# Performance work log

Hardware: AMD Instinct MI355X
Metric: run time of the kernel (lower is better)

The kernel has to match this reference:

```python
import jax, jax.numpy as jnp
import numpy as np

B, S, H, L = 16, 512, 768, 4096

def setup_inputs() -> dict:
    key = jax.random.key(0)
    k1, k2, k3 = jax.random.split(key, 3)
    inputs = jax.random.normal(k1, (B, S, H), dtype=jnp.float32)
    # realistic variable-length masks: each sequence has length in [S//2, S]
    lengths = jax.random.randint(k2, (B,), S // 2, S + 1)
    masks = jnp.arange(S)[None, :] < lengths[:, None]  # [B, S] bool
    # xavier_uniform for Linear(H, L, bias=False): weight shape [L, H]
    limit = float(np.sqrt(6.0 / (H + L)))
    W = jax.random.uniform(k3, (L, H), minval=-limit, maxval=limit, dtype=jnp.float32)
    return {"inputs": inputs, "masks": masks, "W": W}

def reference(inputs, masks, W):
    # scores: Linear(inputs) -> [B,S,L], transposed to [B,L,S]
    scores = jnp.einsum("bsh,lh->bls", inputs, W)
    scores = jnp.where(masks[:, None, :], scores, -jnp.inf)
    attn = jax.nn.softmax(scores, axis=-1)  # over seq dim
    # weighted sum pooling: [B,L,S] @ [B,S,H] -> [B,L,H]
    return jnp.einsum("bls,bsh->blh", attn, inputs)
```

## Files before the change

### kernel.cpp

```cpp
#include <hip/hip_runtime.h>
#include <hip/hip_bf16.h>

#define Bn 16
#define Sn 512
#define Hn 768
#define Ln 4096

typedef __attribute__((ext_vector_type(8))) short bf16x8;
typedef __attribute__((ext_vector_type(4))) float f32x4;

using bf16 = __hip_bfloat16;

constexpr int BL = 64;

constexpr int SM_BYTES = 81920;
constexpr int XS_OFF   = 0;
constexpr int WS_OFF   = 32768;
constexpr int P_OFF    = 0;
constexpr int XT_OFF   = 65536;
constexpr int REDM_OFF = 65536;
constexpr int REDS_OFF = 66048;

typedef const __attribute__((address_space(1))) unsigned int* gas_ptr;
typedef __attribute__((address_space(3))) unsigned int* las_ptr;

__device__ __forceinline__ void gld_lds16(const void* g, void* l) {
  __builtin_amdgcn_global_load_lds((gas_ptr)g, (las_ptr)l, 16, 0, 0);
}

__device__ __forceinline__ unsigned short bfbits(float x) {
  __hip_bfloat16 h = __float2bfloat16(x);
  unsigned short u;
  __builtin_memcpy(&u, &h, 2);
  return u;
}

union Pack8 { bf16 h[8]; uint4 u; };

__device__ inline uint4 cvt8(float4 a, float4 b) {
  Pack8 p;
  p.h[0] = __float2bfloat16(a.x); p.h[1] = __float2bfloat16(a.y);
  p.h[2] = __float2bfloat16(a.z); p.h[3] = __float2bfloat16(a.w);
  p.h[4] = __float2bfloat16(b.x); p.h[5] = __float2bfloat16(b.y);
  p.h[6] = __float2bfloat16(b.z); p.h[7] = __float2bfloat16(b.w);
  return p.u;
}

__global__ __launch_bounds__(256) void convert_x_kernel(
    const float* __restrict__ X, bf16* __restrict__ Xbf, bf16* __restrict__ XT) {
  __shared__ bf16 t[64][72];
  const int tid = threadIdx.x;
  const int b  = blockIdx.z;
  const int s0 = blockIdx.y * 64;
  const int h0 = blockIdx.x * 64;
  const int r = tid >> 2;
  const int p = tid & 3;
  const float* src = X + ((size_t)b * Sn + s0 + r) * Hn + h0 + p * 16;
  float4 a0 = *(const float4*)(src + 0);
  float4 a1 = *(const float4*)(src + 4);
  float4 a2 = *(const float4*)(src + 8);
  float4 a3 = *(const float4*)(src + 12);
  uint4 u0 = cvt8(a0, a1);
  uint4 u1 = cvt8(a2, a3);
  bf16* xb = Xbf + ((size_t)b * Sn + s0 + r) * Hn + h0 + p * 16;
  *(uint4*)(xb)     = u0;
  *(uint4*)(xb + 8) = u1;
  *(uint4*)&t[r][p * 16]     = u0;
  *(uint4*)&t[r][p * 16 + 8] = u1;
  __syncthreads();
  Pack8 o0, o1;
#pragma unroll
  for (int i = 0; i < 8; ++i) {
    o0.h[i] = t[p * 16 + i][r];
    o1.h[i] = t[p * 16 + 8 + i][r];
  }
  bf16* xt = XT + ((size_t)b * Hn + h0 + r) * Sn + s0 + p * 16;
  *(uint4*)(xt)     = o0.u;
  *(uint4*)(xt + 8) = o1.u;
}

__global__ __launch_bounds__(256) void convert_w_kernel(
    const float* __restrict__ W, bf16* __restrict__ Wbf) {
  const size_t i = ((size_t)blockIdx.x * 256 + threadIdx.x) * 8;
  float4 a0 = *(const float4*)(W + i);
  float4 a1 = *(const float4*)(W + i + 4);
  *(uint4*)(Wbf + i) = cvt8(a0, a1);
}

__global__ __launch_bounds__(256, 2) void attn_main_kernel(
    const int* __restrict__ masks,
    const bf16* __restrict__ Xbf, const bf16* __restrict__ XTg,
    const bf16* __restrict__ Wbf, float* __restrict__ out) {
  __shared__ char sm[SM_BYTES];
  const int tid  = threadIdx.x;
  const int w    = tid >> 6;
  const int lane = tid & 63;
  const int col  = lane & 15;
  const int quad = lane >> 4;
  const int lg   = w >> 1;
  const int sg   = w & 1;
  const int b  = blockIdx.x / (Ln / BL);
  const int l0 = (blockIdx.x % (Ln / BL)) * BL;

  float bias_r[16];
  {
    const int* mrow = masks + b * Sn + sg * 256 + col;
#pragma unroll
    for (int nt = 0; nt < 16; ++nt)
      bias_r[nt] = mrow[nt * 16] ? 0.0f : -1e30f;
  }

  const f32x4 zero = {0.f, 0.f, 0.f, 0.f};
  f32x4 acc[2][16];
#pragma unroll
  for (int a = 0; a < 2; ++a)
#pragma unroll
    for (int nt = 0; nt < 16; ++nt) acc[a][nt] = zero;

  for (int k0 = 0; k0 < Hn; k0 += 32) {
    __syncthreads();
    {
      const int r0 = w * 128;
      const bf16* g = Xbf + ((size_t)b * Sn + r0 + (lane >> 2)) * Hn + k0 + (lane & 3) * 8;
#pragma unroll
      for (int i = 0; i < 8; ++i) {
        gld_lds16(g, &sm[XS_OFF + (r0 + i * 16) * 64]);
        g += 16 * Hn;
      }
      const bf16* gw = Wbf + ((size_t)(l0 + w * 16 + (lane >> 2))) * Hn + k0 + (lane & 3) * 8;
      gld_lds16(gw, &sm[WS_OFF + (w * 16) * 64]);
    }
    __syncthreads();
    bf16x8 a0 = *(const bf16x8*)&sm[WS_OFF + (lg * 32 + col) * 64 + quad * 16];
    bf16x8 a1 = *(const bf16x8*)&sm[WS_OFF + (lg * 32 + 16 + col) * 64 + quad * 16];
#pragma unroll
    for (int nt = 0; nt < 16; ++nt) {
      bf16x8 bf_ = *(const bf16x8*)&sm[XS_OFF + (sg * 256 + nt * 16 + col) * 64 + quad * 16];
      acc[0][nt] = __builtin_amdgcn_mfma_f32_16x16x32_bf16(a0, bf_, acc[0][nt], 0, 0, 0);
      acc[1][nt] = __builtin_amdgcn_mfma_f32_16x16x32_bf16(a1, bf_, acc[1][nt], 0, 0, 0);
    }
  }

  float* redm = (float*)&sm[REDM_OFF];
  float* reds = (float*)&sm[REDS_OFF];
  float mx[2][4];
#pragma unroll
  for (int a = 0; a < 2; ++a)
#pragma unroll
    for (int r = 0; r < 4; ++r) mx[a][r] = -3e38f;
#pragma unroll
  for (int a = 0; a < 2; ++a)
#pragma unroll
    for (int nt = 0; nt < 16; ++nt)
#pragma unroll
      for (int r = 0; r < 4; ++r) {
        acc[a][nt][r] += bias_r[nt];
        mx[a][r] = fmaxf(mx[a][r], acc[a][nt][r]);
      }
#pragma unroll
  for (int a = 0; a < 2; ++a)
#pragma unroll
    for (int r = 0; r < 4; ++r) {
      mx[a][r] = fmaxf(mx[a][r], __shfl_xor(mx[a][r], 1, 64));
      mx[a][r] = fmaxf(mx[a][r], __shfl_xor(mx[a][r], 2, 64));
      mx[a][r] = fmaxf(mx[a][r], __shfl_xor(mx[a][r], 4, 64));
      mx[a][r] = fmaxf(mx[a][r], __shfl_xor(mx[a][r], 8, 64));
    }
  if (col == 0) {
#pragma unroll
    for (int a = 0; a < 2; ++a)
#pragma unroll
      for (int r = 0; r < 4; ++r)
        redm[sg * 64 + lg * 32 + a * 16 + quad * 4 + r] = mx[a][r];
  }
  __syncthreads();
  float gmax[2][4], sum[2][4];
#pragma unroll
  for (int a = 0; a < 2; ++a)
#pragma unroll
    for (int r = 0; r < 4; ++r) {
      const int row = lg * 32 + a * 16 + quad * 4 + r;
      gmax[a][r] = fmaxf(redm[row], redm[64 + row]);
      sum[a][r] = 0.f;
    }
#pragma unroll
  for (int a = 0; a < 2; ++a)
#pragma unroll
    for (int nt = 0; nt < 16; ++nt)
#pragma unroll
      for (int r = 0; r < 4; ++r) {
        const float e = __expf(acc[a][nt][r] - gmax[a][r]);
        acc[a][nt][r] = e;
        sum[a][r] += e;
      }
#pragma unroll
  for (int a = 0; a < 2; ++a)
#pragma unroll
    for (int r = 0; r < 4; ++r) {
      sum[a][r] += __shfl_xor(sum[a][r], 1, 64);
      sum[a][r] += __shfl_xor(sum[a][r], 2, 64);
      sum[a][r] += __shfl_xor(sum[a][r], 4, 64);
      sum[a][r] += __shfl_xor(sum[a][r], 8, 64);
    }
  if (col == 0) {
#pragma unroll
    for (int a = 0; a < 2; ++a)
#pragma unroll
      for (int r = 0; r < 4; ++r)
        reds[sg * 64 + lg * 32 + a * 16 + quad * 4 + r] = sum[a][r];
  }
  __syncthreads();
  float rs[2][4];
#pragma unroll
  for (int a = 0; a < 2; ++a)
#pragma unroll
    for (int r = 0; r < 4; ++r) {
      const int row = lg * 32 + a * 16 + quad * 4 + r;
      rs[a][r] = 1.0f / (reds[row] + reds[64 + row]);
    }

  const int pi = col & 1;
#pragma unroll
  for (int a = 0; a < 2; ++a)
#pragma unroll
    for (int t = 0; t < 8; ++t)
#pragma unroll
      for (int r = 0; r < 4; ++r) {
        const float own0 = acc[a][2 * t][r];
        const float own1 = acc[a][2 * t + 1][r];
        const float p0 = __shfl_xor(own0, 1, 64);
        const float p1 = __shfl_xor(own1, 1, 64);
        const float lo = pi ? p1 : own0;
        const float hi = pi ? own1 : p0;
        const unsigned pk = (unsigned)bfbits(lo) | ((unsigned)bfbits(hi) << 16);
        const int nt_w = 2 * t + pi;
        const int row = lg * 32 + a * 16 + quad * 4 + r;
        const int sp = sg * 256 + nt_w * 16 + (col & ~1);
        const int slot = (sp >> 3) ^ (row & 7);
        *(unsigned*)&sm[P_OFF + row * 1024 + slot * 16 + (sp & 7) * 2] = pk;
      }

  for (int n0 = 0; n0 < Hn / 128; ++n0) {
    f32x4 oacc[2][4];
#pragma unroll
    for (int a = 0; a < 2; ++a)
#pragma unroll
      for (int nt = 0; nt < 4; ++nt) oacc[a][nt] = zero;
    for (int s0 = 0; s0 < Sn; s0 += 64) {
      __syncthreads();
      {
        const int r0 = w * 32;
        const int rr = lane >> 3;
        const int cc = lane & 7;
        const bf16* g = XTg + ((size_t)b * Hn + n0 * 128 + r0 + rr) * Sn + s0 + (cc ^ rr) * 8;
#pragma unroll
        for (int i = 0; i < 4; ++i) {
          gld_lds16(g, &sm[XT_OFF + (r0 + i * 8) * 128]);
          g += 8 * Sn;
        }
      }
      __syncthreads();
#pragma unroll
      for (int ks = 0; ks < 2; ++ks) {
        const int chunk = (s0 + ks * 32 + quad * 8) >> 3;
        bf16x8 pa[2];
#pragma unroll
        for (int a = 0; a < 2; ++a) {
          const int row = lg * 32 + a * 16 + col;
          const int slot = chunk ^ (row & 7);
          pa[a] = *(const bf16x8*)&sm[P_OFF + row * 1024 + slot * 16];
        }
#pragma unroll
        for (int nt = 0; nt < 4; ++nt) {
          const int hl = (nt * 2 + sg) * 16 + col;
          const int xslot = (ks * 4 + quad) ^ (hl & 7);
          bf16x8 xb = *(const bf16x8*)&sm[XT_OFF + hl * 128 + xslot * 16];
          oacc[0][nt] = __builtin_amdgcn_mfma_f32_16x16x32_bf16(pa[0], xb, oacc[0][nt], 0, 0, 0);
          oacc[1][nt] = __builtin_amdgcn_mfma_f32_16x16x32_bf16(pa[1], xb, oacc[1][nt], 0, 0, 0);
        }
      }
    }
#pragma unroll
    for (int a = 0; a < 2; ++a)
#pragma unroll
      for (int nt = 0; nt < 4; ++nt) {
        const int h = n0 * 128 + (nt * 2 + sg) * 16 + col;
        const int lbase = l0 + lg * 32 + a * 16 + quad * 4;
#pragma unroll
        for (int r = 0; r < 4; ++r)
          out[((size_t)b * Ln + lbase + r) * Hn + h] = oacc[a][nt][r] * rs[a][r];
      }
  }
}

__global__ __launch_bounds__(256) void attn_fallback_kernel(
    const float* __restrict__ X, const int* __restrict__ masks,
    const float* __restrict__ W, float* __restrict__ out) {
  __shared__ float sc[4][Sn];
  const int wv = threadIdx.x >> 6, lane = threadIdx.x & 63;
  const int gw = blockIdx.x * 4 + wv;
  const int b = gw / Ln, l = gw % Ln;
  float wreg[12];
#pragma unroll
  for (int j = 0; j < 12; ++j) wreg[j] = W[(size_t)l * Hn + j * 64 + lane];
  for (int s = 0; s < Sn; ++s) {
    const float* xr = X + ((size_t)b * Sn + s) * Hn;
    float p = 0.f;
#pragma unroll
    for (int j = 0; j < 12; ++j) p += xr[j * 64 + lane] * wreg[j];
#pragma unroll
    for (int off = 32; off > 0; off >>= 1) p += __shfl_xor(p, off, 64);
    if (lane == 0) sc[wv][s] = p;
  }
  __syncthreads();
  float m = -3e38f;
#pragma unroll
  for (int i = 0; i < 8; ++i) {
    const int s = lane * 8 + i;
    const float v = sc[wv][s] + (masks[b * Sn + s] ? 0.f : -1e30f);
    sc[wv][s] = v;
    m = fmaxf(m, v);
  }
#pragma unroll
  for (int off = 32; off > 0; off >>= 1) m = fmaxf(m, __shfl_xor(m, off, 64));
  __syncthreads();
  float sum = 0.f;
#pragma unroll
  for (int i = 0; i < 8; ++i) {
    const int s = lane * 8 + i;
    const float e = __expf(sc[wv][s] - m);
    sc[wv][s] = e;
    sum += e;
  }
#pragma unroll
  for (int off = 32; off > 0; off >>= 1) sum += __shfl_xor(sum, off, 64);
  const float rs = 1.0f / sum;
  __syncthreads();
  float o[12];
#pragma unroll
  for (int j = 0; j < 12; ++j) o[j] = 0.f;
  for (int s = 0; s < Sn; ++s) {
    const float p = sc[wv][s];
    const float* xr = X + ((size_t)b * Sn + s) * Hn;
#pragma unroll
    for (int j = 0; j < 12; ++j) o[j] += p * xr[j * 64 + lane];
  }
#pragma unroll
  for (int j = 0; j < 12; ++j)
    out[((size_t)b * Ln + l) * Hn + j * 64 + lane] = o[j] * rs;
}

extern "C" void kernel_launch(void* const* d_in, const int* in_sizes, int n_in,
                              void* d_out, int out_size, void* d_ws, size_t ws_size,
                              hipStream_t stream) {
  const float* X     = (const float*)d_in[0];
  const int*   masks = (const int*)d_in[1];
  const float* W     = (const float*)d_in[2];
  float* out = (float*)d_out;

  const size_t need = ((size_t)2 * Bn * Sn * Hn + (size_t)Ln * Hn) * sizeof(bf16);
  if (ws_size >= need) {
    bf16* Xbf = (bf16*)d_ws;
    bf16* XT  = Xbf + (size_t)Bn * Sn * Hn;
    bf16* Wbf = XT  + (size_t)Bn * Sn * Hn;
    convert_x_kernel<<<dim3(Hn / 64, Sn / 64, Bn), 256, 0, stream>>>(X, Xbf, XT);
    convert_w_kernel<<<dim3((Ln * Hn) / 2048), 256, 0, stream>>>(W, Wbf);
    attn_main_kernel<<<dim3(Bn * (Ln / BL)), 256, 0, stream>>>(masks, Xbf, XT, Wbf, out);
  } else {
    attn_fallback_kernel<<<dim3(Bn * Ln / 4), 256, 0, stream>>>(X, masks, W, out);
  }
}
```

Baseline: 374.8 us.

## Double-buffer score GEMM, swizzle LDS, re-split warps, prefetch XT via registers

```diff
diff --git a/kernel.cpp b/kernel.cpp
--- a/kernel.cpp
+++ b/kernel.cpp
@@ -14,12 +14,11 @@
 constexpr int BL = 64;
 
 constexpr int SM_BYTES = 81920;
-constexpr int XS_OFF   = 0;
-constexpr int WS_OFF   = 32768;
+constexpr int PH2_BUF  = 36864;
 constexpr int P_OFF    = 0;
 constexpr int XT_OFF   = 65536;
-constexpr int REDM_OFF = 65536;
-constexpr int REDS_OFF = 66048;
+constexpr int REDM_OFF = 73728;
+constexpr int REDS_OFF = 74752;
 
 typedef const __attribute__((address_space(1))) unsigned int* gas_ptr;
 typedef __attribute__((address_space(3))) unsigned int* las_ptr;
@@ -99,66 +98,84 @@
   const int quad = lane >> 4;
   const int lg   = w >> 1;
   const int sg   = w & 1;
-  const int b  = blockIdx.x / (Ln / BL);
-  const int l0 = (blockIdx.x % (Ln / BL)) * BL;
-
-  float bias_r[16];
+  const int vb = (blockIdx.x & 7) * 128 + (blockIdx.x >> 3);
+  const int b  = vb >> 6;
+  const int l0 = (vb & 63) * BL;
+
+  float bias_r[8];
   {
-    const int* mrow = masks + b * Sn + sg * 256 + col;
-#pragma unroll
-    for (int nt = 0; nt < 16; ++nt)
+    const int* mrow = masks + b * Sn + w * 128 + col;
+#pragma unroll
+    for (int nt = 0; nt < 8; ++nt)
       bias_r[nt] = mrow[nt * 16] ? 0.0f : -1e30f;
   }
 
   const f32x4 zero = {0.f, 0.f, 0.f, 0.f};
-  f32x4 acc[2][16];
-#pragma unroll
-  for (int a = 0; a < 2; ++a)
-#pragma unroll
-    for (int nt = 0; nt < 16; ++nt) acc[a][nt] = zero;
-
+  f32x4 acc[4][8];
+#pragma unroll
+  for (int a = 0; a < 4; ++a)
+#pragma unroll
+    for (int nt = 0; nt < 8; ++nt) acc[a][nt] = zero;
+
+  const int rr2 = lane >> 2;
+  const int cc2 = lane & 3;
+  const int swk = (cc2 ^ (rr2 & 3)) * 8;
+
+  auto stage2 = [&](int p, int k0) {
+    const bf16* gx = Xbf + ((size_t)b * Sn + w * 128 + rr2) * Hn + k0 + swk;
+    char* dx = sm + p * PH2_BUF + (w * 128) * 64;
+#pragma unroll
+    for (int i = 0; i < 8; ++i) {
+      gld_lds16(gx, dx);
+      gx += 16 * Hn;
+      dx += 16 * 64;
+    }
+    const bf16* gw = Wbf + ((size_t)(l0 + w * 16 + rr2)) * Hn + k0 + swk;
+    gld_lds16(gw, sm + p * PH2_BUF + 32768 + (w * 16) * 64);
+  };
+
+  stage2(0, 0);
+  __syncthreads();
+  int p = 0;
+  const int swr = (quad ^ (col & 3)) * 16;
   for (int k0 = 0; k0 < Hn; k0 += 32) {
+    if (k0 + 32 < Hn) stage2(p ^ 1, k0 + 32);
+    const char* xs = sm + p * PH2_BUF;
+    const char* ws = sm + p * PH2_BUF + 32768;
+    bf16x8 aF[4], bF[8];
+#pragma unroll
+    for (int a = 0; a < 4; ++a)
+      aF[a] = *(const bf16x8*)(ws + (a * 16 + col) * 64 + swr);
+#pragma unroll
+    for (int nt = 0; nt < 8; ++nt)
+      bF[nt] = *(const bf16x8*)(xs + (w * 128 + nt * 16 + col) * 64 + swr);
+#pragma unroll
+    for (int nt = 0; nt < 8; ++nt)
+#pragma unroll
+      for (int a = 0; a < 4; ++a)
+        acc[a][nt] = __builtin_amdgcn_mfma_f32_16x16x32_bf16(aF[a], bF[nt], acc[a][nt], 0, 0, 0);
     __syncthreads();
-    {
-      const int r0 = w * 128;
-      const bf16* g = Xbf + ((size_t)b * Sn + r0 + (lane >> 2)) * Hn + k0 + (lane & 3) * 8;
-#pragma unroll
-      for (int i = 0; i < 8; ++i) {
-        gld_lds16(g, &sm[XS_OFF + (r0 + i * 16) * 64]);
-        g += 16 * Hn;
-      }
-      const bf16* gw = Wbf + ((size_t)(l0 + w * 16 + (lane >> 2))) * Hn + k0 + (lane & 3) * 8;
-      gld_lds16(gw, &sm[WS_OFF + (w * 16) * 64]);
-    }
-    __syncthreads();
-    bf16x8 a0 = *(const bf16x8*)&sm[WS_OFF + (lg * 32 + col) * 64 + quad * 16];
-    bf16x8 a1 = *(const bf16x8*)&sm[WS_OFF + (lg * 32 + 16 + col) * 64 + quad * 16];
-#pragma unroll
-    for (int nt = 0; nt < 16; ++nt) {
-      bf16x8 bf_ = *(const bf16x8*)&sm[XS_OFF + (sg * 256 + nt * 16 + col) * 64 + quad * 16];
-      acc[0][nt] = __builtin_amdgcn_mfma_f32_16x16x32_bf16(a0, bf_, acc[0][nt], 0, 0, 0);
-      acc[1][nt] = __builtin_amdgcn_mfma_f32_16x16x32_bf16(a1, bf_, acc[1][nt], 0, 0, 0);
-    }
+    p ^= 1;
   }
 
   float* redm = (float*)&sm[REDM_OFF];
   float* reds = (float*)&sm[REDS_OFF];
-  float mx[2][4];
-#pragma unroll
-  for (int a = 0; a < 2; ++a)
+  float mx[4][4];
+#pragma unroll
+  for (int a = 0; a < 4; ++a)
 #pragma unroll
     for (int r = 0; r < 4; ++r) mx[a][r] = -3e38f;
 #pragma unroll
-  for (int a = 0; a < 2; ++a)
-#pragma unroll
-    for (int nt = 0; nt < 16; ++nt)
+  for (int a = 0; a < 4; ++a)
+#pragma unroll
+    for (int nt = 0; nt < 8; ++nt)
 #pragma unroll
       for (int r = 0; r < 4; ++r) {
         acc[a][nt][r] += bias_r[nt];
         mx[a][r] = fmaxf(mx[a][r], acc[a][nt][r]);
       }
 #pragma unroll
-  for (int a = 0; a < 2; ++a)
+  for (int a = 0; a < 4; ++a)
 #pragma unroll
     for (int r = 0; r < 4; ++r) {
       mx[a][r] = fmaxf(mx[a][r], __shfl_xor(mx[a][r], 1, 64));
@@ -168,25 +185,26 @@
     }
   if (col == 0) {
 #pragma unroll
-    for (int a = 0; a < 2; ++a)
+    for (int a = 0; a < 4; ++a)
 #pragma unroll
       for (int r = 0; r < 4; ++r)
-        redm[sg * 64 + lg * 32 + a * 16 + quad * 4 + r] = mx[a][r];
-  }
-  __syncthreads();
-  float gmax[2][4], sum[2][4];
-#pragma unroll
-  for (int a = 0; a < 2; ++a)
+        redm[w * 64 + a * 16 + quad * 4 + r] = mx[a][r];
+  }
+  __syncthreads();
+  float gmax[4][4], sum[4][4];
+#pragma unroll
+  for (int a = 0; a < 4; ++a)
 #pragma unroll
     for (int r = 0; r < 4; ++r) {
-      const int row = lg * 32 + a * 16 + quad * 4 + r;
-      gmax[a][r] = fmaxf(redm[row], redm[64 + row]);
+      const int row = a * 16 + quad * 4 + r;
+      gmax[a][r] = fmaxf(fmaxf(redm[row], redm[64 + row]),
+                         fmaxf(redm[128 + row], redm[192 + row]));
       sum[a][r] = 0.f;
     }
 #pragma unroll
-  for (int a = 0; a < 2; ++a)
-#pragma unroll
-    for (int nt = 0; nt < 16; ++nt)
+  for (int a = 0; a < 4; ++a)
+#pragma unroll
+    for (int nt = 0; nt < 8; ++nt)
 #pragma unroll
       for (int r = 0; r < 4; ++r) {
         const float e = __expf(acc[a][nt][r] - gmax[a][r]);
@@ -194,7 +212,7 @@
         sum[a][r] += e;
       }
 #pragma unroll
-  for (int a = 0; a < 2; ++a)
+  for (int a = 0; a < 4; ++a)
 #pragma unroll
     for (int r = 0; r < 4; ++r) {
       sum[a][r] += __shfl_xor(sum[a][r], 1, 64);
@@ -204,26 +222,39 @@
     }
   if (col == 0) {
 #pragma unroll
-    for (int a = 0; a < 2; ++a)
+    for (int a = 0; a < 4; ++a)
 #pragma unroll
       for (int r = 0; r < 4; ++r)
-        reds[sg * 64 + lg * 32 + a * 16 + quad * 4 + r] = sum[a][r];
-  }
-  __syncthreads();
-  float rs[2][4];
-#pragma unroll
-  for (int a = 0; a < 2; ++a)
+        reds[w * 64 + a * 16 + quad * 4 + r] = sum[a][r];
+  }
+  __syncthreads();
+  float rs[4][4];
+#pragma unroll
+  for (int a = 0; a < 4; ++a)
 #pragma unroll
     for (int r = 0; r < 4; ++r) {
-      const int row = lg * 32 + a * 16 + quad * 4 + r;
-      rs[a][r] = 1.0f / (reds[row] + reds[64 + row]);
-    }
+      const int row = a * 16 + quad * 4 + r;
+      rs[a][r] = 1.0f / (reds[row] + reds[64 + row] + reds[128 + row] + reds[192 + row]);
+    }
+
+  const int rr5 = lane >> 3;
+  const int cc5 = lane & 7;
+  uint4 xtr[4];
+  auto load_xt = [&](int n0, int s0) {
+    const bf16* g = XTg + ((size_t)b * Hn + n0 * 128 + w * 32 + rr5) * Sn + s0 + cc5 * 8;
+#pragma unroll
+    for (int i = 0; i < 4; ++i) {
+      xtr[i] = *(const uint4*)g;
+      g += 8 * Sn;
+    }
+  };
+  load_xt(0, 0);
 
   const int pi = col & 1;
 #pragma unroll
-  for (int a = 0; a < 2; ++a)
-#pragma unroll
-    for (int t = 0; t < 8; ++t)
+  for (int a = 0; a < 4; ++a)
+#pragma unroll
+    for (int t = 0; t < 4; ++t)
 #pragma unroll
       for (int r = 0; r < 4; ++r) {
         const float own0 = acc[a][2 * t][r];
@@ -234,8 +265,8 @@
         const float hi = pi ? own1 : p0;
         const unsigned pk = (unsigned)bfbits(lo) | ((unsigned)bfbits(hi) << 16);
         const int nt_w = 2 * t + pi;
-        const int row = lg * 32 + a * 16 + quad * 4 + r;
-        const int sp = sg * 256 + nt_w * 16 + (col & ~1);
+        const int row = a * 16 + quad * 4 + r;
+        const int sp = w * 128 + nt_w * 16 + (col & ~1);
         const int slot = (sp >> 3) ^ (row & 7);
         *(unsigned*)&sm[P_OFF + row * 1024 + slot * 16 + (sp & 7) * 2] = pk;
       }
@@ -248,18 +279,15 @@
       for (int nt = 0; nt < 4; ++nt) oacc[a][nt] = zero;
     for (int s0 = 0; s0 < Sn; s0 += 64) {
       __syncthreads();
-      {
-        const int r0 = w * 32;
-        const int rr = lane >> 3;
-        const int cc = lane & 7;
-        const bf16* g = XTg + ((size_t)b * Hn + n0 * 128 + r0 + rr) * Sn + s0 + (cc ^ rr) * 8;
-#pragma unroll
-        for (int i = 0; i < 4; ++i) {
-          gld_lds16(g, &sm[XT_OFF + (r0 + i * 8) * 128]);
-          g += 8 * Sn;
-        }
-      }
+#pragma unroll
+      for (int i = 0; i < 4; ++i)
+        *(uint4*)&sm[XT_OFF + (w * 32 + i * 8 + rr5) * 128 + ((cc5 ^ rr5) * 16)] = xtr[i];
       __syncthreads();
+      if (!((n0 == Hn / 128 - 1) && (s0 + 64 == Sn))) {
+        int ns0 = s0 + 64, nn0 = n0;
+        if (ns0 == Sn) { ns0 = 0; ++nn0; }
+        load_xt(nn0, ns0);
+      }
 #pragma unroll
       for (int ks = 0; ks < 2; ++ks) {
         const int chunk = (s0 + ks * 32 + quad * 8) >> 3;
@@ -288,7 +316,7 @@
         const int lbase = l0 + lg * 32 + a * 16 + quad * 4;
 #pragma unroll
         for (int r = 0; r < 4; ++r)
-          out[((size_t)b * Ln + lbase + r) * Hn + h] = oacc[a][nt][r] * rs[a][r];
+          out[((size_t)b * Ln + lbase + r) * Hn + h] = oacc[a][nt][r] * rs[lg * 2 + a][r];
       }
   }
 }
```

Result: slower. 511.3 us (+36.4%).

## Halve L tile to 32 rows, shrink LDS, raise occupancy and swizzle block order

Applied to the files above, without the earlier changes.

```diff
diff --git a/kernel.cpp b/kernel.cpp
--- a/kernel.cpp
+++ b/kernel.cpp
@@ -11,15 +11,15 @@
 
 using bf16 = __hip_bfloat16;
 
-constexpr int BL = 64;
-
-constexpr int SM_BYTES = 81920;
+constexpr int BL = 32;
+
+constexpr int SM_BYTES = 49664;
 constexpr int XS_OFF   = 0;
 constexpr int WS_OFF   = 32768;
 constexpr int P_OFF    = 0;
-constexpr int XT_OFF   = 65536;
-constexpr int REDM_OFF = 65536;
-constexpr int REDS_OFF = 66048;
+constexpr int XT_OFF   = 32768;
+constexpr int REDM_OFF = 49152;
+constexpr int REDS_OFF = 49408;
 
 typedef const __attribute__((address_space(1))) unsigned int* gas_ptr;
 typedef __attribute__((address_space(3))) unsigned int* las_ptr;
@@ -87,7 +87,7 @@
   *(uint4*)(Wbf + i) = cvt8(a0, a1);
 }
 
-__global__ __launch_bounds__(256, 2) void attn_main_kernel(
+__global__ __launch_bounds__(256, 3) void attn_main_kernel(
     const int* __restrict__ masks,
     const bf16* __restrict__ Xbf, const bf16* __restrict__ XTg,
     const bf16* __restrict__ Wbf, float* __restrict__ out) {
@@ -99,8 +99,9 @@
   const int quad = lane >> 4;
   const int lg   = w >> 1;
   const int sg   = w & 1;
-  const int b  = blockIdx.x / (Ln / BL);
-  const int l0 = (blockIdx.x % (Ln / BL)) * BL;
+  const int vb = (blockIdx.x & 7) * 256 + (blockIdx.x >> 3);
+  const int b  = vb >> 7;
+  const int l0 = (vb & 127) * BL;
 
   float bias_r[16];
   {
@@ -111,11 +112,9 @@
   }
 
   const f32x4 zero = {0.f, 0.f, 0.f, 0.f};
-  f32x4 acc[2][16];
-#pragma unroll
-  for (int a = 0; a < 2; ++a)
-#pragma unroll
-    for (int nt = 0; nt < 16; ++nt) acc[a][nt] = zero;
+  f32x4 acc[16];
+#pragma unroll
+  for (int nt = 0; nt < 16; ++nt) acc[nt] = zero;
 
   for (int k0 = 0; k0 < Hn; k0 += 32) {
     __syncthreads();
@@ -127,125 +126,103 @@
         gld_lds16(g, &sm[XS_OFF + (r0 + i * 16) * 64]);
         g += 16 * Hn;
       }
-      const bf16* gw = Wbf + ((size_t)(l0 + w * 16 + (lane >> 2))) * Hn + k0 + (lane & 3) * 8;
-      gld_lds16(gw, &sm[WS_OFF + (w * 16) * 64]);
+      if (w < 2) {
+        const bf16* gw = Wbf + ((size_t)(l0 + w * 16 + (lane >> 2))) * Hn + k0 + (lane & 3) * 8;
+        gld_lds16(gw, &sm[WS_OFF + (w * 16) * 64]);
+      }
     }
     __syncthreads();
-    bf16x8 a0 = *(const bf16x8*)&sm[WS_OFF + (lg * 32 + col) * 64 + quad * 16];
-    bf16x8 a1 = *(const bf16x8*)&sm[WS_OFF + (lg * 32 + 16 + col) * 64 + quad * 16];
+    bf16x8 aF = *(const bf16x8*)&sm[WS_OFF + (lg * 16 + col) * 64 + quad * 16];
 #pragma unroll
     for (int nt = 0; nt < 16; ++nt) {
-      bf16x8 bf_ = *(const bf16x8*)&sm[XS_OFF + (sg * 256 + nt * 16 + col) * 64 + quad * 16];
-      acc[0][nt] = __builtin_amdgcn_mfma_f32_16x16x32_bf16(a0, bf_, acc[0][nt], 0, 0, 0);
-      acc[1][nt] = __builtin_amdgcn_mfma_f32_16x16x32_bf16(a1, bf_, acc[1][nt], 0, 0, 0);
+      bf16x8 bF = *(const bf16x8*)&sm[XS_OFF + (sg * 256 + nt * 16 + col) * 64 + quad * 16];
+      acc[nt] = __builtin_amdgcn_mfma_f32_16x16x32_bf16(aF, bF, acc[nt], 0, 0, 0);
     }
   }
 
   float* redm = (float*)&sm[REDM_OFF];
   float* reds = (float*)&sm[REDS_OFF];
-  float mx[2][4];
-#pragma unroll
-  for (int a = 0; a < 2; ++a)
-#pragma unroll
-    for (int r = 0; r < 4; ++r) mx[a][r] = -3e38f;
-#pragma unroll
-  for (int a = 0; a < 2; ++a)
-#pragma unroll
-    for (int nt = 0; nt < 16; ++nt)
-#pragma unroll
-      for (int r = 0; r < 4; ++r) {
-        acc[a][nt][r] += bias_r[nt];
-        mx[a][r] = fmaxf(mx[a][r], acc[a][nt][r]);
-      }
-#pragma unroll
-  for (int a = 0; a < 2; ++a)
+  float mx[4];
+#pragma unroll
+  for (int r = 0; r < 4; ++r) mx[r] = -3e38f;
+#pragma unroll
+  for (int nt = 0; nt < 16; ++nt)
 #pragma unroll
     for (int r = 0; r < 4; ++r) {
-      mx[a][r] = fmaxf(mx[a][r], __shfl_xor(mx[a][r], 1, 64));
-      mx[a][r] = fmaxf(mx[a][r], __shfl_xor(mx[a][r], 2, 64));
-      mx[a][r] = fmaxf(mx[a][r], __shfl_xor(mx[a][r], 4, 64));
-      mx[a][r] = fmaxf(mx[a][r], __shfl_xor(mx[a][r], 8, 64));
-    }
+      acc[nt][r] += bias_r[nt];
+      mx[r] = fmaxf(mx[r], acc[nt][r]);
+    }
+#pragma unroll
+  for (int r = 0; r < 4; ++r) {
+    mx[r] = fmaxf(mx[r], __shfl_xor(mx[r], 1, 64));
+    mx[r] = fmaxf(mx[r], __shfl_xor(mx[r], 2, 64));
+    mx[r] = fmaxf(mx[r], __shfl_xor(mx[r], 4, 64));
+    mx[r] = fmaxf(mx[r], __shfl_xor(mx[r], 8, 64));
+  }
   if (col == 0) {
 #pragma unroll
-    for (int a = 0; a < 2; ++a)
-#pragma unroll
-      for (int r = 0; r < 4; ++r)
-        redm[sg * 64 + lg * 32 + a * 16 + quad * 4 + r] = mx[a][r];
-  }
-  __syncthreads();
-  float gmax[2][4], sum[2][4];
-#pragma unroll
-  for (int a = 0; a < 2; ++a)
+    for (int r = 0; r < 4; ++r)
+      redm[sg * 32 + lg * 16 + quad * 4 + r] = mx[r];
+  }
+  __syncthreads();
+  float gmax[4], sum[4];
+#pragma unroll
+  for (int r = 0; r < 4; ++r) {
+    const int row = lg * 16 + quad * 4 + r;
+    gmax[r] = fmaxf(redm[row], redm[32 + row]);
+    sum[r] = 0.f;
+  }
+#pragma unroll
+  for (int nt = 0; nt < 16; ++nt)
 #pragma unroll
     for (int r = 0; r < 4; ++r) {
-      const int row = lg * 32 + a * 16 + quad * 4 + r;
-      gmax[a][r] = fmaxf(redm[row], redm[64 + row]);
-      sum[a][r] = 0.f;
-    }
-#pragma unroll
-  for (int a = 0; a < 2; ++a)
-#pragma unroll
-    for (int nt = 0; nt < 16; ++nt)
-#pragma unroll
-      for (int r = 0; r < 4; ++r) {
-        const float e = __expf(acc[a][nt][r] - gmax[a][r]);
-        acc[a][nt][r] = e;
-        sum[a][r] += e;
-      }
-#pragma unroll
-  for (int a = 0; a < 2; ++a)
+      const float e = __expf(acc[nt][r] - gmax[r]);
+      acc[nt][r] = e;
+      sum[r] += e;
+    }
+#pragma unroll
+  for (int r = 0; r < 4; ++r) {
+    sum[r] += __shfl_xor(sum[r], 1, 64);
+    sum[r] += __shfl_xor(sum[r], 2, 64);
+    sum[r] += __shfl_xor(sum[r], 4, 64);
+    sum[r] += __shfl_xor(sum[r], 8, 64);
+  }
+  if (col == 0) {
+#pragma unroll
+    for (int r = 0; r < 4; ++r)
+      reds[sg * 32 + lg * 16 + quad * 4 + r] = sum[r];
+  }
+  __syncthreads();
+  float rs[4];
+#pragma unroll
+  for (int r = 0; r < 4; ++r) {
+    const int row = lg * 16 + quad * 4 + r;
+    rs[r] = 1.0f / (reds[row] + reds[32 + row]);
+  }
+
+  const int pi = col & 1;
+#pragma unroll
+  for (int t = 0; t < 8; ++t)
 #pragma unroll
     for (int r = 0; r < 4; ++r) {
-      sum[a][r] += __shfl_xor(sum[a][r], 1, 64);
-      sum[a][r] += __shfl_xor(sum[a][r], 2, 64);
-      sum[a][r] += __shfl_xor(sum[a][r], 4, 64);
-      sum[a][r] += __shfl_xor(sum[a][r], 8, 64);
-    }
-  if (col == 0) {
-#pragma unroll
-    for (int a = 0; a < 2; ++a)
-#pragma unroll
-      for (int r = 0; r < 4; ++r)
-        reds[sg * 64 + lg * 32 + a * 16 + quad * 4 + r] = sum[a][r];
-  }
-  __syncthreads();
-  float rs[2][4];
-#pragma unroll
-  for (int a = 0; a < 2; ++a)
-#pragma unroll
-    for (int r = 0; r < 4; ++r) {
-      const int row = lg * 32 + a * 16 + quad * 4 + r;
-      rs[a][r] = 1.0f / (reds[row] + reds[64 + row]);
-    }
-
-  const int pi = col & 1;
-#pragma unroll
-  for (int a = 0; a < 2; ++a)
-#pragma unroll
-    for (int t = 0; t < 8; ++t)
-#pragma unroll
-      for (int r = 0; r < 4; ++r) {
-        const float own0 = acc[a][2 * t][r];
-        const float own1 = acc[a][2 * t + 1][r];
-        const float p0 = __shfl_xor(own0, 1, 64);
-        const float p1 = __shfl_xor(own1, 1, 64);
-        const float lo = pi ? p1 : own0;
-        const float hi = pi ? own1 : p0;
-        const unsigned pk = (unsigned)bfbits(lo) | ((unsigned)bfbits(hi) << 16);
-        const int nt_w = 2 * t + pi;
-        const int row = lg * 32 + a * 16 + quad * 4 + r;
-        const int sp = sg * 256 + nt_w * 16 + (col & ~1);
-        const int slot = (sp >> 3) ^ (row & 7);
-        *(unsigned*)&sm[P_OFF + row * 1024 + slot * 16 + (sp & 7) * 2] = pk;
-      }
+      const float own0 = acc[2 * t][r];
+      const float own1 = acc[2 * t + 1][r];
+      const float p0 = __shfl_xor(own0, 1, 64);
+      const float p1 = __shfl_xor(own1, 1, 64);
+      const float lo = pi ? p1 : own0;
+      const float hi = pi ? own1 : p0;
+      const unsigned pk = (unsigned)bfbits(lo) | ((unsigned)bfbits(hi) << 16);
+      const int nt_w = 2 * t + pi;
+      const int row = lg * 16 + quad * 4 + r;
+      const int sp = sg * 256 + nt_w * 16 + (col & ~1);
+      const int slot = (sp >> 3) ^ (row & 7);
+      *(unsigned*)&sm[P_OFF + row * 1024 + slot * 16 + (sp & 7) * 2] = pk;
+    }
 
   for (int n0 = 0; n0 < Hn / 128; ++n0) {
-    f32x4 oacc[2][4];
-#pragma unroll
-    for (int a = 0; a < 2; ++a)
-#pragma unroll
-      for (int nt = 0; nt < 4; ++nt) oacc[a][nt] = zero;
+    f32x4 oacc[4];
+#pragma unroll
+    for (int nt = 0; nt < 4; ++nt) oacc[nt] = zero;
     for (int s0 = 0; s0 < Sn; s0 += 64) {
       __syncthreads();
       {
@@ -263,33 +240,26 @@
 #pragma unroll
       for (int ks = 0; ks < 2; ++ks) {
         const int chunk = (s0 + ks * 32 + quad * 8) >> 3;
-        bf16x8 pa[2];
-#pragma unroll
-        for (int a = 0; a < 2; ++a) {
-          const int row = lg * 32 + a * 16 + col;
-          const int slot = chunk ^ (row & 7);
-          pa[a] = *(const bf16x8*)&sm[P_OFF + row * 1024 + slot * 16];
-        }
+        const int row = lg * 16 + col;
+        const int slot = chunk ^ (row & 7);
+        bf16x8 pa = *(const bf16x8*)&sm[P_OFF + row * 1024 + slot * 16];
 #pragma unroll
         for (int nt = 0; nt < 4; ++nt) {
           const int hl = (nt * 2 + sg) * 16 + col;
           const int xslot = (ks * 4 + quad) ^ (hl & 7);
           bf16x8 xb = *(const bf16x8*)&sm[XT_OFF + hl * 128 + xslot * 16];
-          oacc[0][nt] = __builtin_amdgcn_mfma_f32_16x16x32_bf16(pa[0], xb, oacc[0][nt], 0, 0, 0);
-          oacc[1][nt] = __builtin_amdgcn_mfma_f32_16x16x32_bf16(pa[1], xb, oacc[1][nt], 0, 0, 0);
+          oacc[nt] = __builtin_amdgcn_mfma_f32_16x16x32_bf16(pa, xb, oacc[nt], 0, 0, 0);
         }
       }
     }
 #pragma unroll
-    for (int a = 0; a < 2; ++a)
-#pragma unroll
-      for (int nt = 0; nt < 4; ++nt) {
-        const int h = n0 * 128 + (nt * 2 + sg) * 16 + col;
-        const int lbase = l0 + lg * 32 + a * 16 + quad * 4;
-#pragma unroll
-        for (int r = 0; r < 4; ++r)
-          out[((size_t)b * Ln + lbase + r) * Hn + h] = oacc[a][nt][r] * rs[a][r];
-      }
+    for (int nt = 0; nt < 4; ++nt) {
+      const int h = n0 * 128 + (nt * 2 + sg) * 16 + col;
+      const int lbase = l0 + lg * 16 + quad * 4;
+#pragma unroll
+      for (int r = 0; r < 4; ++r)
+        out[((size_t)b * Ln + lbase + r) * Hn + h] = oacc[nt][r] * rs[r];
+    }
   }
 }
 
```

Result: slower. 415.7 us (+10.9%).

## Double-buffer score GEMM LDS staging and remap block order across XCDs

Applied to the files above, without the earlier changes.

```diff
diff --git a/kernel.cpp b/kernel.cpp
--- a/kernel.cpp
+++ b/kernel.cpp
@@ -13,13 +13,13 @@
 
 constexpr int BL = 64;
 
-constexpr int SM_BYTES = 81920;
-constexpr int XS_OFF   = 0;
-constexpr int WS_OFF   = 32768;
-constexpr int P_OFF    = 0;
-constexpr int XT_OFF   = 65536;
-constexpr int REDM_OFF = 65536;
-constexpr int REDS_OFF = 66048;
+constexpr int SM_BYTES  = 81920;
+constexpr int PH2_BUF   = 36864;
+constexpr int WS_OFF_IN = 32768;
+constexpr int P_OFF     = 0;
+constexpr int XT_OFF    = 65536;
+constexpr int REDM_OFF  = 73728;
+constexpr int REDS_OFF  = 74240;
 
 typedef const __attribute__((address_space(1))) unsigned int* gas_ptr;
 typedef __attribute__((address_space(3))) unsigned int* las_ptr;
@@ -99,8 +99,9 @@
   const int quad = lane >> 4;
   const int lg   = w >> 1;
   const int sg   = w & 1;
-  const int b  = blockIdx.x / (Ln / BL);
-  const int l0 = (blockIdx.x % (Ln / BL)) * BL;
+  const int vb = (blockIdx.x & 7) * 128 + (blockIdx.x >> 3);
+  const int b  = vb >> 6;
+  const int l0 = (vb & 63) * BL;
 
   float bias_r[16];
   {
@@ -117,29 +118,52 @@
 #pragma unroll
     for (int nt = 0; nt < 16; ++nt) acc[a][nt] = zero;
 
-  for (int k0 = 0; k0 < Hn; k0 += 32) {
-    __syncthreads();
-    {
-      const int r0 = w * 128;
-      const bf16* g = Xbf + ((size_t)b * Sn + r0 + (lane >> 2)) * Hn + k0 + (lane & 3) * 8;
-#pragma unroll
-      for (int i = 0; i < 8; ++i) {
-        gld_lds16(g, &sm[XS_OFF + (r0 + i * 16) * 64]);
-        g += 16 * Hn;
-      }
-      const bf16* gw = Wbf + ((size_t)(l0 + w * 16 + (lane >> 2))) * Hn + k0 + (lane & 3) * 8;
-      gld_lds16(gw, &sm[WS_OFF + (w * 16) * 64]);
-    }
-    __syncthreads();
-    bf16x8 a0 = *(const bf16x8*)&sm[WS_OFF + (lg * 32 + col) * 64 + quad * 16];
-    bf16x8 a1 = *(const bf16x8*)&sm[WS_OFF + (lg * 32 + 16 + col) * 64 + quad * 16];
-#pragma unroll
-    for (int nt = 0; nt < 16; ++nt) {
-      bf16x8 bf_ = *(const bf16x8*)&sm[XS_OFF + (sg * 256 + nt * 16 + col) * 64 + quad * 16];
-      acc[0][nt] = __builtin_amdgcn_mfma_f32_16x16x32_bf16(a0, bf_, acc[0][nt], 0, 0, 0);
-      acc[1][nt] = __builtin_amdgcn_mfma_f32_16x16x32_bf16(a1, bf_, acc[1][nt], 0, 0, 0);
-    }
-  }
+  const int rr2 = lane >> 2;
+  const int cc2 = (lane & 3) * 8;
+
+#define STAGE2(BUFOFF, K0)                                                         \
+  {                                                                                \
+    const bf16* gx = Xbf + ((size_t)b * Sn + w * 128 + rr2) * Hn + (K0) + cc2;     \
+    char* dx = sm + (BUFOFF) + (w * 128) * 64;                                     \
+    _Pragma("unroll")                                                              \
+    for (int i = 0; i < 8; ++i) {                                                  \
+      gld_lds16(gx, dx);                                                           \
+      gx += 16 * Hn;                                                               \
+      dx += 16 * 64;                                                               \
+    }                                                                              \
+    const bf16* gw = Wbf + ((size_t)(l0 + w * 16 + rr2)) * Hn + (K0) + cc2;        \
+    gld_lds16(gw, sm + (BUFOFF) + WS_OFF_IN + (w * 16) * 64);                      \
+  }
+
+#define PH2_COMPUTE(BUFOFF)                                                        \
+  {                                                                                \
+    const char* xs = sm + (BUFOFF);                                                \
+    const char* ws = sm + (BUFOFF) + WS_OFF_IN;                                    \
+    bf16x8 a0 = *(const bf16x8*)&ws[(lg * 32 + col) * 64 + quad * 16];             \
+    bf16x8 a1 = *(const bf16x8*)&ws[(lg * 32 + 16 + col) * 64 + quad * 16];        \
+    _Pragma("unroll")                                                              \
+    for (int nt = 0; nt < 16; ++nt) {                                              \
+      bf16x8 bf_ = *(const bf16x8*)&xs[(sg * 256 + nt * 16 + col) * 64 + quad * 16]; \
+      acc[0][nt] = __builtin_amdgcn_mfma_f32_16x16x32_bf16(a0, bf_, acc[0][nt], 0, 0, 0); \
+      acc[1][nt] = __builtin_amdgcn_mfma_f32_16x16x32_bf16(a1, bf_, acc[1][nt], 0, 0, 0); \
+    }                                                                              \
+  }
+
+  STAGE2(0, 0);
+  asm volatile("s_waitcnt vmcnt(0)" ::: "memory");
+  __builtin_amdgcn_s_barrier();
+  for (int k0 = 0; k0 < Hn; k0 += 64) {
+    STAGE2(PH2_BUF, k0 + 32);
+    PH2_COMPUTE(0);
+    asm volatile("s_waitcnt vmcnt(0)" ::: "memory");
+    __builtin_amdgcn_s_barrier();
+    if (k0 + 64 < Hn) STAGE2(0, k0 + 64);
+    PH2_COMPUTE(PH2_BUF);
+    asm volatile("s_waitcnt vmcnt(0)" ::: "memory");
+    __builtin_amdgcn_s_barrier();
+  }
+#undef STAGE2
+#undef PH2_COMPUTE
 
   float* redm = (float*)&sm[REDM_OFF];
   float* reds = (float*)&sm[REDS_OFF];
```

Result: no change. 372.4 us (-0.7%).
